# Kernel optimization log

Hardware: AMD Instinct MI355X
Metric: run time of the kernel (lower is better)

The kernel has to match this reference:

```python
import jax, jax.numpy as jnp
import numpy as np

T, H = 2048, 1024
NH, NKV, HD = 8, 2, 128
E, TOPK, NG, TKG = 16, 4, 4, 2
F, FS = 1024, 1024
EPS = 1e-6
ROUTED_SCALE = 2.0
THETA = 10000.0


def _rmsnorm(x, w):
    return x * jax.lax.rsqrt(jnp.mean(x * x, axis=-1, keepdims=True) + EPS) * w


def setup_inputs() -> dict:
    key = jax.random.key(0)
    ks = jax.random.split(key, 12)
    s = 0.02
    return {
        "hidden_states": jax.random.normal(ks[0], (T, H), jnp.float32),
        "residual": jax.random.normal(ks[1], (T, H), jnp.float32),
        "position_ids": jnp.arange(T, dtype=jnp.int32),
        "ln1_w": jnp.ones((H,), jnp.float32),
        "qkv_w": s * jax.random.normal(ks[2], (H, (NH + 2 * NKV) * HD), jnp.float32),
        "qnorm_w": jnp.ones((HD,), jnp.float32),
        "knorm_w": jnp.ones((HD,), jnp.float32),
        "dense_w": s * jax.random.normal(ks[3], (NH * HD, H), jnp.float32),
        "ln2_w": jnp.ones((H,), jnp.float32),
        "gate_w": s * jax.random.normal(ks[4], (H, E), jnp.float32),
        "expert_bias": 0.1 * jax.random.normal(ks[5], (E,), jnp.float32),
        "w13": s * jax.random.normal(ks[6], (E, H, 2 * F), jnp.float32),
        "w2": s * jax.random.normal(ks[7], (E, F, H), jnp.float32),
        "ws_gate_up": s * jax.random.normal(ks[8], (H, 2 * FS), jnp.float32),
        "ws_down": s * jax.random.normal(ks[9], (FS, H), jnp.float32),
    }


def block_forward(hidden_states, residual, position_ids, ln1_w, qkv_w, qnorm_w,
                  knorm_w, dense_w, ln2_w, gate_w, expert_bias, w13, w2,
                  ws_gate_up, ws_down):
    # fused add + RMSNorm (input_layernorm with residual)
    resid = hidden_states + residual
    h = _rmsnorm(resid, ln1_w)

    # --- attention ---
    qkv = h @ qkv_w  # [T, (NH+2*NKV)*HD]
    q = qkv[:, : NH * HD].reshape(T, NH, HD)
    k = qkv[:, NH * HD : (NH + NKV) * HD].reshape(T, NKV, HD)
    v = qkv[:, (NH + NKV) * HD :].reshape(T, NKV, HD)
    q = _rmsnorm(q, qnorm_w)  # qk-norm per head_dim
    k = _rmsnorm(k, knorm_w)

    # neox-style RoPE over full head_dim
    inv_freq = 1.0 / (THETA ** (jnp.arange(0, HD, 2, dtype=jnp.float32) / HD))
    ang = position_ids.astype(jnp.float32)[:, None] * inv_freq[None, :]  # [T, HD/2]
    cos = jnp.cos(ang)[:, None, :]
    sin = jnp.sin(ang)[:, None, :]

    def rope(x):
        x1, x2 = x[..., : HD // 2], x[..., HD // 2 :]
        return jnp.concatenate([x1 * cos - x2 * sin, x2 * cos + x1 * sin], axis=-1)

    q, k = rope(q), rope(k)
    rep = NH // NKV
    kr = jnp.repeat(k, rep, axis=1)  # [T, NH, HD]
    vr = jnp.repeat(v, rep, axis=1)

    scores = jnp.einsum("qhd,khd->hqk", q, kr) * (HD ** -0.5)
    causal = jnp.tril(jnp.ones((T, T), bool))
    scores = jnp.where(causal[None], scores, jnp.finfo(scores.dtype).min)
    probs = jax.nn.softmax(scores, axis=-1)
    ctx = jnp.einsum("hqk,khd->qhd", probs, vr).reshape(T, NH * HD)
    attn_out = ctx @ dense_w

    # fused add + RMSNorm (post_attention_layernorm)
    resid2 = attn_out + resid
    h2 = _rmsnorm(resid2, ln2_w)

    # --- MoE router: sigmoid scoring + correction bias, grouped top-k ---
    logits = h2.astype(jnp.float32) @ gate_w  # router in fp32
    s_scores = jax.nn.sigmoid(logits)  # [T, E]
    sfc = s_scores + expert_bias[None, :]
    gview = sfc.reshape(T, NG, E // NG)
    gscores = jax.lax.top_k(gview, 2)[0].sum(-1)  # sum of top-2 per group
    gidx = jax.lax.top_k(gscores, TKG)[1]  # [T, TKG]
    gmask = jax.nn.one_hot(gidx, NG, dtype=sfc.dtype).sum(1)  # [T, NG]
    smask = jnp.repeat(gmask, E // NG, axis=1)  # [T, E]
    masked = jnp.where(smask > 0, sfc, -jnp.inf)
    topk_idx = jax.lax.top_k(masked, TOPK)[1]  # [T, TOPK]
    topk_w = jnp.take_along_axis(s_scores, topk_idx, axis=1)  # weights w/o bias
    topk_w = topk_w / (topk_w.sum(-1, keepdims=True) + 1e-20)  # renormalize
    combine = (jax.nn.one_hot(topk_idx, E, dtype=topk_w.dtype) * topk_w[..., None]).sum(1)  # [T, E]

    # routed experts (dense-over-experts reference for the grouped GEMM)
    gu = jnp.einsum("th,ehf->tef", h2, w13)  # [T, E, 2F]
    g, u = gu[..., :F], gu[..., F:]
    act = jax.nn.silu(g) * u
    y = jnp.einsum("tef,efh->teh", act, w2)
    routed = jnp.einsum("teh,te->th", y, combine) * ROUTED_SCALE

    # shared expert (SwiGLU MLP)
    su = h2 @ ws_gate_up
    shared = (jax.nn.silu(su[:, :FS]) * su[:, FS:]) @ ws_down

    mlp_out = routed + shared
    return mlp_out, resid2


def reference(hidden_states, residual, position_ids, ln1_w, qkv_w, qnorm_w,
              knorm_w, dense_w, ln2_w, gate_w, expert_bias, w13, w2,
              ws_gate_up, ws_down):
    return block_forward(hidden_states, residual, position_ids, ln1_w, qkv_w,
                         qnorm_w, knorm_w, dense_w, ln2_w, gate_w, expert_bias,
                         w13, w2, ws_gate_up, ws_down)
```

## Files before the change

kernel.cpp:

```cpp
#include <hip/hip_runtime.h>
#include <hip/hip_bf16.h>


#define T_TOK 2048
#define H_DIM 1024
#define NHEAD 8
#define NKVH 2
#define HDIM 128
#define QKV_DIM 1536
#define E_EXP 16
#define TOPKE 4
#define F_DIM 1024
#define FS_DIM 1024
#define NPAIR (T_TOK*TOPKE)
#define EPS_F 1e-6f

#define DEV __device__ __forceinline__

typedef __attribute__((ext_vector_type(4))) float f32x4;
typedef __attribute__((ext_vector_type(8))) short s16x8;

DEV float us2f(unsigned short u){ return __uint_as_float(((unsigned int)u)<<16); }
DEV unsigned short f2us(float f){
  __hip_bfloat16 b = __float2bfloat16(f);
  unsigned short u; __builtin_memcpy(&u,&b,2); return u;
}

DEV void gl2lds16(const void* g, void* l){
  __builtin_amdgcn_global_load_lds(
      (const __attribute__((address_space(1))) void*)g,
      (__attribute__((address_space(3))) void*)l, 16, 0, 0);
}

DEV int crow(int qt){ int a=qt>>2, b=qt&3; return (a+1)*(2*a+b); }

DEV float bred_sum(float v, float* sm){
  #pragma unroll
  for(int o=32;o>0;o>>=1) v += __shfl_down(v,o);
  int w = threadIdx.x>>6, l = threadIdx.x&63;
  __syncthreads();
  if(l==0) sm[w]=v;
  __syncthreads();
  return sm[0]+sm[1]+sm[2]+sm[3];
}

__global__ __launch_bounds__(256) void k_cvt_t(const float* __restrict__ in,
    unsigned short* __restrict__ out, int Kd, int Nd){
  const int z = blockIdx.z;
  const int kb = blockIdx.y*32, nb = blockIdx.x*32;
  __shared__ float Lt[32][33];
  const int tid = threadIdx.x;
  const int r = tid>>3, c4 = (tid&7)*4;
  const float* src = in + (long long)z*Kd*Nd + (long long)(kb+r)*Nd + nb + c4;
  float4 v = *(const float4*)src;
  Lt[r][c4+0]=v.x; Lt[r][c4+1]=v.y; Lt[r][c4+2]=v.z; Lt[r][c4+3]=v.w;
  __syncthreads();
  ushort4 o;
  o.x = f2us(Lt[c4+0][r]); o.y = f2us(Lt[c4+1][r]);
  o.z = f2us(Lt[c4+2][r]); o.w = f2us(Lt[c4+3][r]);
  *(ushort4*)(out + (long long)z*Nd*Kd + (long long)(nb+r)*Kd + kb + c4) = o;
}

template<bool GROUPED, bool GATHER>
__global__ __launch_bounds__(256) void gemm_mfma(
    const unsigned short* __restrict__ A, int lda,
    const unsigned short* __restrict__ Bt, int ldbt, long long bstride,
    unsigned short* __restrict__ C, int ldc,
    const int* __restrict__ rowidx, const int* __restrict__ grpoff,
    int Mdense, int K){
  const int z = blockIdx.z;
  const int rb = GROUPED ? grpoff[z] : 0;
  const int re = GROUPED ? grpoff[z+1] : Mdense;
  const int m0 = rb + blockIdx.y*128;
  if(m0 >= re) return;
  const int n0 = blockIdx.x*128;
  const unsigned short* Bz = Bt + (long long)z*bstride;

  __shared__ unsigned short As[128][32];
  __shared__ unsigned short Bs[128][32];

  const int tid = threadIdx.x;
  const int s0 = tid, s1 = tid+256;
  int gr0 = m0 + (s0>>2), gr1 = m0 + (s1>>2);
  if(GROUPED){ gr0 = min(gr0, re-1); gr1 = min(gr1, re-1); }
  if(GATHER){ gr0 = rowidx[gr0]; gr1 = rowidx[gr1]; }
  const unsigned short* ag0 = A + (long long)gr0*lda + (s0&3)*8;
  const unsigned short* ag1 = A + (long long)gr1*lda + (s1&3)*8;
  const unsigned short* bg0 = Bz + (long long)(n0 + (s0>>2))*ldbt + (s0&3)*8;
  const unsigned short* bg1 = Bz + (long long)(n0 + (s1>>2))*ldbt + (s1&3)*8;
  char* asb = (char*)&As[0][0];
  char* bsb = (char*)&Bs[0][0];
  const int wb = (tid & 192)*16;

  const int w = tid>>6, lane = tid&63;
  const int wm = (w>>1)*64, wn = (w&1)*64;
  const int fr = lane&15, q8 = (lane>>4)*8;

  f32x4 zero = {0.f,0.f,0.f,0.f};
  f32x4 acc[4][4];
  #pragma unroll
  for(int mi=0;mi<4;mi++)
    #pragma unroll
    for(int ni=0;ni<4;ni++) acc[mi][ni]=zero;

  for(int k0=0;k0<K;k0+=32){
    __syncthreads();
    gl2lds16(ag0 + k0, asb + wb);
    gl2lds16(ag1 + k0, asb + 4096 + wb);
    gl2lds16(bg0 + k0, bsb + wb);
    gl2lds16(bg1 + k0, bsb + 4096 + wb);
    __syncthreads();
    s16x8 af[4], bf[4];
    #pragma unroll
    for(int mi=0;mi<4;mi++) af[mi] = *(const s16x8*)&As[wm+mi*16+fr][q8];
    #pragma unroll
    for(int ni=0;ni<4;ni++) bf[ni] = *(const s16x8*)&Bs[wn+ni*16+fr][q8];
    #pragma unroll
    for(int mi=0;mi<4;mi++)
      #pragma unroll
      for(int ni=0;ni<4;ni++)
        acc[mi][ni] = __builtin_amdgcn_mfma_f32_16x16x32_bf16(af[mi], bf[ni], acc[mi][ni], 0,0,0);
  }
  const int q4 = (lane>>4)*4;
  #pragma unroll
  for(int mi=0;mi<4;mi++)
    #pragma unroll
    for(int ni=0;ni<4;ni++){
      const int col = n0 + wn + ni*16 + fr;
      #pragma unroll
      for(int r=0;r<4;r++){
        const int row = m0 + wm + mi*16 + q4 + r;
        if(row < re) C[(long long)row*ldc + col] = f2us(acc[mi][ni][r]);
      }
    }
}

__global__ __launch_bounds__(256) void k_silu(const unsigned short* __restrict__ gu,
    unsigned short* __restrict__ act){
  const int r = blockIdx.x, c = threadIdx.x*4;
  const ushort4 g4 = *(const ushort4*)(gu + (long long)r*2048 + c);
  const ushort4 u4 = *(const ushort4*)(gu + (long long)r*2048 + 1024 + c);
  float g[4] = {us2f(g4.x),us2f(g4.y),us2f(g4.z),us2f(g4.w)};
  float u[4] = {us2f(u4.x),us2f(u4.y),us2f(u4.z),us2f(u4.w)};
  ushort4 o;
  o.x = f2us((g[0]/(1.f+__expf(-g[0])))*u[0]);
  o.y = f2us((g[1]/(1.f+__expf(-g[1])))*u[1]);
  o.z = f2us((g[2]/(1.f+__expf(-g[2])))*u[2]);
  o.w = f2us((g[3]/(1.f+__expf(-g[3])))*u[3]);
  *(ushort4*)(act + (long long)r*1024 + c) = o;
}

__global__ __launch_bounds__(256) void k_add_rmsnorm(const float* __restrict__ hs,
    const float* __restrict__ rs, const float* __restrict__ w,
    float* __restrict__ resid, float* __restrict__ h){
  int t = blockIdx.x, tid = threadIdx.x;
  __shared__ float sm[4];
  const long base = (long)t*H_DIM;
  float x[4]; float ss = 0.f;
  #pragma unroll
  for(int i=0;i<4;i++){
    int c = tid + i*256;
    float v = hs[base+c] + rs[base+c];
    x[i]=v; resid[base+c]=v; ss += v*v;
  }
  float tot = bred_sum(ss, sm);
  float rms = rsqrtf(tot/(float)H_DIM + EPS_F);
  #pragma unroll
  for(int i=0;i<4;i++){
    int c = tid + i*256;
    h[base+c] = x[i]*rms*w[c];
  }
}

template<int EPI_ADD>
__global__ __launch_bounds__(256) void gemm_f32(
    const float* __restrict__ A, int lda,
    const float* __restrict__ B, int ldb,
    float* __restrict__ C, int ldc,
    const float* __restrict__ D, int M, int K){
  const int m0 = blockIdx.y*128;
  const int n0 = blockIdx.x*64;
  __shared__ float As[16][132];
  __shared__ float Bs[16][65];
  float acc[8][4];
  #pragma unroll
  for(int i=0;i<8;i++)
    #pragma unroll
    for(int j=0;j<4;j++) acc[i][j]=0.f;
  const int tid = threadIdx.x;
  const int tx = tid & 15, ty = tid >> 4;
  const int ar = tid >> 1, ac = (tid & 1)*8;
  const int brr = tid >> 4, bc = (tid & 15)*4;
  const float* Aptr = A + (long long)(m0+ar)*lda;
  for(int k0=0;k0<K;k0+=16){
    float4 a0 = *(const float4*)(Aptr + k0 + ac);
    float4 a1 = *(const float4*)(Aptr + k0 + ac + 4);
    float4 bv = *(const float4*)(B + (long long)(k0+brr)*ldb + n0 + bc);
    __syncthreads();
    As[ac+0][ar]=a0.x; As[ac+1][ar]=a0.y; As[ac+2][ar]=a0.z; As[ac+3][ar]=a0.w;
    As[ac+4][ar]=a1.x; As[ac+5][ar]=a1.y; As[ac+6][ar]=a1.z; As[ac+7][ar]=a1.w;
    Bs[brr][bc+0]=bv.x; Bs[brr][bc+1]=bv.y; Bs[brr][bc+2]=bv.z; Bs[brr][bc+3]=bv.w;
    __syncthreads();
    #pragma unroll
    for(int kk=0;kk<16;kk++){
      float a[8], b[4];
      #pragma unroll
      for(int i=0;i<8;i++) a[i]=As[kk][ty*8+i];
      #pragma unroll
      for(int j=0;j<4;j++) b[j]=Bs[kk][tx*4+j];
      #pragma unroll
      for(int i=0;i<8;i++)
        #pragma unroll
        for(int j=0;j<4;j++) acc[i][j] = fmaf(a[i], b[j], acc[i][j]);
    }
  }
  #pragma unroll
  for(int i=0;i<8;i++){
    int r = m0 + ty*8 + i;
    float* crow = C + (long long)r*ldc + n0 + tx*4;
    float4 v = make_float4(acc[i][0],acc[i][1],acc[i][2],acc[i][3]);
    if(EPI_ADD){
      const float4 d = *(const float4*)(D + (long long)r*ldc + n0 + tx*4);
      v.x+=d.x; v.y+=d.y; v.z+=d.z; v.w+=d.w;
    }
    *(float4*)crow = v;
  }
}

__global__ __launch_bounds__(64) void k_qkv_post(const float* __restrict__ qkv,
    const float* __restrict__ qw, const float* __restrict__ kw,
    const int* __restrict__ pos,
    float* __restrict__ qb, float* __restrict__ kb, float* __restrict__ vb){
  int slot = blockIdx.x, t = blockIdx.y, lane = threadIdx.x;
  const float* x = qkv + (long long)t*QKV_DIM + slot*HDIM;
  float x0 = x[lane], x1 = x[lane+64];
  if(slot < 10){
    float ss = x0*x0 + x1*x1;
    #pragma unroll
    for(int o=32;o>0;o>>=1) ss += __shfl_xor(ss,o);
    float rms = rsqrtf(ss/(float)HDIM + EPS_F);
    const float* w = (slot<8)? qw : kw;
    float n0 = x0*rms*w[lane];
    float n1 = x1*rms*w[lane+64];
    float p = (float)pos[t];
    float invf = __expf(-((float)lane/64.f)*9.210340371976184f);
    float ang = p*invf;
    float s = sinf(ang), c = cosf(ang);
    float o0 = n0*c - n1*s;
    float o1 = n1*c + n0*s;
    float* dst = (slot<8)? (qb + ((long long)slot*T_TOK + t)*HDIM)
                         : (kb + ((long long)(slot-8)*T_TOK + t)*HDIM);
    dst[lane]=o0; dst[lane+64]=o1;
  } else {
    float* dst = vb + ((long long)(slot-10)*T_TOK + t)*HDIM;
    dst[lane]=x0; dst[lane+64]=x1;
  }
}

#define FBQ 32
#define FBK 128
__global__ __launch_bounds__(256,2) void k_flash(const float* __restrict__ qb,
    const float* __restrict__ kb, const float* __restrict__ vb,
    float* __restrict__ ctx, float* __restrict__ Op1, float* __restrict__ Op2,
    float* __restrict__ Ml){
  const int b = blockIdx.x;
  const int u0 = (17*b)>>1, u1 = (17*(b+1))>>1;
  const int tid = threadIdx.x;
  const int lane = tid & 63;
  const int w = tid >> 6;
  const int tx = tid & 31;
  const int ty = tid >> 5;
  const int fsw = tx & 7;

  __shared__ float4 smem4[4096];
  char*  smem = (char*)smem4;
  float* Ksf  = (float*)smem;
  float* Psf  = (float*)(smem + 49152);

  const float scale = 0.08838834764831845f;

  int h = u0/544;
  int r = u0 - h*544;
  int qt = 0;
  while(qt < 63 && crow(qt+1) <= r) qt++;
  int kt = r - crow(qt);

  int u = u0;
  while(u < u1){
    const int nkt = (qt>>2) + 1;
    const int q0 = qt * FBQ;
    const int kv = h >> 2;
    const float* kbase = kb + (long long)kv*T_TOK*HDIM;
    const float* vbase = vb + (long long)kv*T_TOK*HDIM;
    const float* qrow0 = qb + ((long long)h*T_TOK + q0 + ty*4)*HDIM;
    const int segN = min(nkt - kt, u1 - u);
    const int ktEnd = kt + segN;

    float m_[4], l_[4], O[4][4];
    #pragma unroll
    for(int qi=0;qi<4;qi++){
      m_[qi] = -1e30f; l_[qi] = 0.f;
      #pragma unroll
      for(int j=0;j<4;j++) O[qi][j] = 0.f;
    }

    for(; kt<ktEnd; kt++){
      const int k0 = kt * FBK;
      __syncthreads();
      {
        const float* kcur = kbase + (long long)k0*HDIM;
        #pragma unroll
        for(int i=0;i<16;i++){
          const int rbase = (w<<5) + (i<<1);
          const int f = (i>>1) & 7;
          const float* src = kcur + (long long)(rbase + (lane>>5))*HDIM
                                  + (((lane&31)^f)<<2);
          gl2lds16(src, smem + rbase*512);
        }
      }
      __syncthreads();

      float s[4][4];
      #pragma unroll
      for(int qi=0;qi<4;qi++)
        #pragma unroll
        for(int ki=0;ki<4;ki++) s[qi][ki] = 0.f;

      #pragma unroll 2
      for(int dc=0; dc<32; dc++){
        float4 qv[4];
        #pragma unroll
        for(int qi=0;qi<4;qi++) qv[qi] = *(const float4*)(qrow0 + qi*HDIM + dc*4);
        float4 kf[4];
        #pragma unroll
        for(int ki=0;ki<4;ki++)
          kf[ki] = *(const float4*)&Ksf[(size_t)(4*tx+ki)*128 + ((dc ^ fsw)<<2)];
        #pragma unroll
        for(int qi=0;qi<4;qi++)
          #pragma unroll
          for(int ki=0;ki<4;ki++){
            s[qi][ki] = fmaf(qv[qi].x, kf[ki].x, s[qi][ki]);
            s[qi][ki] = fmaf(qv[qi].y, kf[ki].y, s[qi][ki]);
            s[qi][ki] = fmaf(qv[qi].z, kf[ki].z, s[qi][ki]);
            s[qi][ki] = fmaf(qv[qi].w, kf[ki].w, s[qi][ki]);
          }
      }

      const bool last = (kt == nkt-1);
      float rm[4];
      #pragma unroll
      for(int qi=0;qi<4;qi++){
        #pragma unroll
        for(int ki=0;ki<4;ki++){
          float v = s[qi][ki]*scale;
          if(last && (k0 + 4*tx + ki > q0 + ty*4 + qi)) v = -1e30f;
          s[qi][ki] = v;
        }
        rm[qi] = fmaxf(fmaxf(s[qi][0],s[qi][1]), fmaxf(s[qi][2],s[qi][3]));
      }
      #pragma unroll
      for(int o=1;o<32;o<<=1){
        #pragma unroll
        for(int qi=0;qi<4;qi++) rm[qi] = fmaxf(rm[qi], __shfl_xor(rm[qi], o));
      }
      float a_[4], rs[4];
      #pragma unroll
      for(int qi=0;qi<4;qi++){
        float mn = fmaxf(m_[qi], rm[qi]);
        a_[qi] = __expf(m_[qi] - mn);
        m_[qi] = mn;
        float rr = 0.f;
        #pragma unroll
        for(int ki=0;ki<4;ki++){ s[qi][ki] = __expf(s[qi][ki] - mn); rr += s[qi][ki]; }
        rs[qi] = rr;
      }
      #pragma unroll
      for(int o=1;o<32;o<<=1){
        #pragma unroll
        for(int qi=0;qi<4;qi++) rs[qi] += __shfl_xor(rs[qi], o);
      }
      #pragma unroll
      for(int qi=0;qi<4;qi++){
        l_[qi] = l_[qi]*a_[qi] + rs[qi];
        #pragma unroll
        for(int j=0;j<4;j++) O[qi][j] *= a_[qi];
      }

      __syncthreads();
      #pragma unroll
      for(int ki=0;ki<4;ki++){
        float4 pv;
        pv.x = s[0][ki]; pv.y = s[1][ki]; pv.z = s[2][ki]; pv.w = s[3][ki];
        *(float4*)&Psf[(size_t)(4*tx+ki)*32 + ((ty ^ fsw)<<2)] = pv;
      }
      __syncthreads();

      const float* vcur = vbase + (long long)k0*HDIM + tx*4;
      #pragma unroll 4
      for(int k=0;k<FBK;k++){
        float4 p4 = *(const float4*)&Psf[(size_t)k*32 + ((ty ^ ((k>>2)&7))<<2)];
        float4 vv = *(const float4*)(vcur + (size_t)k*HDIM);
        O[0][0]=fmaf(p4.x,vv.x,O[0][0]); O[0][1]=fmaf(p4.x,vv.y,O[0][1]);
        O[0][2]=fmaf(p4.x,vv.z,O[0][2]); O[0][3]=fmaf(p4.x,vv.w,O[0][3]);
        O[1][0]=fmaf(p4.y,vv.x,O[1][0]); O[1][1]=fmaf(p4.y,vv.y,O[1][1]);
        O[1][2]=fmaf(p4.y,vv.z,O[1][2]); O[1][3]=fmaf(p4.y,vv.w,O[1][3]);
        O[2][0]=fmaf(p4.z,vv.x,O[2][0]); O[2][1]=fmaf(p4.z,vv.y,O[2][1]);
        O[2][2]=fmaf(p4.z,vv.z,O[2][2]); O[2][3]=fmaf(p4.z,vv.w,O[2][3]);
        O[3][0]=fmaf(p4.w,vv.x,O[3][0]); O[3][1]=fmaf(p4.w,vv.y,O[3][1]);
        O[3][2]=fmaf(p4.w,vv.z,O[3][2]); O[3][3]=fmaf(p4.w,vv.w,O[3][3]);
      }
    }

    {
      const int R = (h<<6) + qt;
      const int S = h*544 + crow(qt);
      const int bS = (2*S+1)/17;
      const int j = b - bS;
      #pragma unroll
      for(int qi=0;qi<4;qi++){
        const int row = ty*4 + qi;
        float4 o4 = make_float4(O[qi][0],O[qi][1],O[qi][2],O[qi][3]);
        if(j==0){
          *(float4*)(ctx + (long long)(q0+row)*(NHEAD*HDIM) + h*HDIM + tx*4) = o4;
        } else if(j==1){
          *(float4*)(Op1 + (long long)R*4096 + row*128 + tx*4) = o4;
        } else {
          *(float4*)(Op2 + (long long)R*4096 + row*128 + tx*4) = o4;
        }
        if(tx==0){
          Ml[((R*3+j)<<6) + row*2 + 0] = m_[qi];
          Ml[((R*3+j)<<6) + row*2 + 1] = l_[qi];
        }
      }
    }

    u += segN;
    if(ktEnd == nkt){ kt = 0; qt++; if(qt == 64){ qt = 0; h++; } }
    else kt = ktEnd;
  }
}

__global__ __launch_bounds__(256) void k_fmerge(float* __restrict__ ctx,
    const float* __restrict__ Op1, const float* __restrict__ Op2,
    const float* __restrict__ Ml){
  const int wv = threadIdx.x>>6, lane = threadIdx.x&63;
  const int gr = blockIdx.x*4 + wv;
  const int R = gr>>5, q = gr&31;
  const int h = R>>6, qt = R&63;
  const int nkt = (qt>>2)+1;
  const int S = h*544 + crow(qt);
  const int bS = (2*S+1)/17;
  const int bE = (2*(S+nkt-1)+1)/17;
  const int parts = bE - bS + 1;
  float* dst = ctx + (long long)(qt*32+q)*(NHEAD*HDIM) + h*HDIM + lane*2;
  float2 o0 = *(float2*)dst;
  const float* mlb = Ml + ((R*3)<<6) + q*2;
  const float m0 = mlb[0], l0 = mlb[1];
  float ox, oy;
  if(parts == 1){
    float inv = 1.f/l0;
    ox = o0.x*inv; oy = o0.y*inv;
  } else {
    const float m1 = mlb[64], l1 = mlb[65];
    float2 o1 = *(const float2*)(Op1 + (long long)R*4096 + q*128 + lane*2);
    if(parts == 2){
      float mx = fmaxf(m0,m1);
      float a0 = __expf(m0-mx), a1 = __expf(m1-mx);
      float inv = 1.f/(l0*a0 + l1*a1);
      ox = (o0.x*a0 + o1.x*a1)*inv;
      oy = (o0.y*a0 + o1.y*a1)*inv;
    } else {
      const float m2 = mlb[128], l2 = mlb[129];
      float2 o2 = *(const float2*)(Op2 + (long long)R*4096 + q*128 + lane*2);
      float mx = fmaxf(fmaxf(m0,m1),m2);
      float a0 = __expf(m0-mx), a1 = __expf(m1-mx), a2 = __expf(m2-mx);
      float inv = 1.f/(l0*a0 + l1*a1 + l2*a2);
      ox = (o0.x*a0 + o1.x*a1 + o2.x*a2)*inv;
      oy = (o0.y*a0 + o1.y*a1 + o2.y*a2)*inv;
    }
  }
  dst[0] = ox; dst[1] = oy;
}

__global__ __launch_bounds__(256) void k_rms2(const float* __restrict__ r2,
    const float* __restrict__ w, float* __restrict__ h2f,
    unsigned short* __restrict__ h2b){
  int t = blockIdx.x, tid = threadIdx.x;
  __shared__ float sm[4];
  const long base = (long)t*H_DIM;
  float x[4]; float ss=0.f;
  #pragma unroll
  for(int i=0;i<4;i++){
    int c = tid+i*256;
    float v = r2[base+c];
    x[i]=v; ss += v*v;
  }
  float tot = bred_sum(ss, sm);
  float rms = rsqrtf(tot/(float)H_DIM + EPS_F);
  #pragma unroll
  for(int i=0;i<4;i++){
    int c = tid+i*256;
    float v = x[i]*rms*w[c];
    h2f[base+c] = v;
    h2b[base+c] = f2us(v);
  }
}

__global__ __launch_bounds__(256) void k_router(const float* __restrict__ h2,
    const float* __restrict__ gw, const float* __restrict__ eb,
    int* __restrict__ topk_idx, float* __restrict__ topk_w, int* __restrict__ counts){
  int t = blockIdx.x, tid = threadIdx.x;
  int e = tid & 15, seg = tid >> 4;
  const float* hrow = h2 + (long long)t*H_DIM;
  float part = 0.f;
  #pragma unroll 4
  for(int i=0;i<64;i++){
    int hh = seg*64 + i;
    part += hrow[hh]*gw[hh*E_EXP + e];
  }
  __shared__ float pm[16][17];
  __shared__ float sS[16], sfc[16];
  pm[seg][e] = part;
  __syncthreads();
  if(tid < 16){
    float l = 0.f;
    #pragma unroll
    for(int s=0;s<16;s++) l += pm[s][tid];
    float sg = 1.f/(1.f+expf(-l));
    sS[tid]=sg; sfc[tid]=sg+eb[tid];
  }
  __syncthreads();
  if(tid==0){
    float gs[4];
    #pragma unroll
    for(int g=0; g<4; g++){
      float m1=-1e30f, m2=-1e30f;
      for(int j=0;j<4;j++){
        float v=sfc[g*4+j];
        if(v>m1){ m2=m1; m1=v; } else if(v>m2){ m2=v; }
      }
      gs[g]=m1+m2;
    }
    int g1=0; for(int g=1;g<4;g++) if(gs[g]>gs[g1]) g1=g;
    int g2=-1; for(int g=0;g<4;g++){ if(g==g1) continue; if(g2<0||gs[g]>gs[g2]) g2=g; }
    bool taken[16];
    #pragma unroll
    for(int i=0;i<16;i++) taken[i]=false;
    int idx[4];
    for(int j=0;j<4;j++){
      int best=-1; float bv=-1e30f;
      for(int i=0;i<16;i++){
        int g=i>>2;
        if(g!=g1 && g!=g2) continue;
        if(taken[i]) continue;
        if(best<0 || sfc[i]>bv){ best=i; bv=sfc[i]; }
      }
      taken[best]=true; idx[j]=best;
    }
    float w[4]; float s=0.f;
    #pragma unroll
    for(int j=0;j<4;j++){ w[j]=sS[idx[j]]; s+=w[j]; }
    s += 1e-20f;
    #pragma unroll
    for(int j=0;j<4;j++){
      topk_idx[t*4+j]=idx[j];
      topk_w[t*4+j]=w[j]/s;
      atomicAdd(&counts[idx[j]],1);
    }
  }
}

__global__ void k_zero(int* __restrict__ counts){ if(threadIdx.x<16) counts[threadIdx.x]=0; }

__global__ void k_scan(const int* __restrict__ counts, int* __restrict__ offs, int* __restrict__ cursor){
  if(threadIdx.x==0){
    int s=0;
    for(int e2=0;e2<16;e2++){ offs[e2]=s; cursor[e2]=s; s+=counts[e2]; }
    offs[16]=s;
  }
}

__global__ __launch_bounds__(256) void k_scatter(const int* __restrict__ topk_idx,
    int* __restrict__ cursor, int* __restrict__ pair_tok, int* __restrict__ tok2pair){
  int i = blockIdx.x*256 + threadIdx.x;
  int e = topk_idx[i];
  int pos = atomicAdd(&cursor[e],1);
  pair_tok[pos] = i>>2;
  tok2pair[i] = pos;
}

__global__ __launch_bounds__(256) void k_combine(const unsigned short* __restrict__ y,
    const unsigned short* __restrict__ sout, const int* __restrict__ tok2pair,
    const float* __restrict__ topk_w, float* __restrict__ out0){
  int t = blockIdx.x, tid = threadIdx.x;
  int p[4]; float w[4];
  #pragma unroll
  for(int j=0;j<4;j++){ p[j]=tok2pair[t*4+j]; w[j]=topk_w[t*4+j]*2.0f; }
  const long base = (long)t*H_DIM;
  #pragma unroll
  for(int i=0;i<4;i++){
    int c = tid + i*256;
    float v = us2f(sout[base+c]);
    #pragma unroll
    for(int j=0;j<4;j++) v += w[j]*us2f(y[(long long)p[j]*H_DIM + c]);
    out0[base+c] = v;
  }
}

extern "C" void kernel_launch(void* const* d_in, const int* in_sizes, int n_in,
                              void* d_out, int out_size, void* d_ws, size_t ws_size,
                              hipStream_t stream) {
  const float* hs   = (const float*)d_in[0];
  const float* rsd  = (const float*)d_in[1];
  const int*   pos  = (const int*)d_in[2];
  const float* ln1  = (const float*)d_in[3];
  const float* qkvw = (const float*)d_in[4];
  const float* qnw  = (const float*)d_in[5];
  const float* knw  = (const float*)d_in[6];
  const float* dw   = (const float*)d_in[7];
  const float* ln2  = (const float*)d_in[8];
  const float* gw   = (const float*)d_in[9];
  const float* eb   = (const float*)d_in[10];
  const float* w13  = (const float*)d_in[11];
  const float* w2   = (const float*)d_in[12];
  const float* wsgu = (const float*)d_in[13];
  const float* wsd  = (const float*)d_in[14];
  float* out0 = (float*)d_out;
  float* out1 = out0 + (size_t)T_TOK*H_DIM;

  char* W = (char*)d_ws;
  float* resid = (float*)(W + 0);
  float* h     = (float*)(W + 8388608);
  float* ctx   = h;
  float* qkv   = (float*)(W + 16777216);
  float* qb    = (float*)(W + 29360128);
  float* h2f   = (float*)(W + 37748736);
  float* kb    = (float*)(W + 46137344);
  float* vb    = (float*)(W + 48234496);
  float* Op1   = (float*)(W + 16777216);
  float* Ml    = (float*)(W + 25165824);
  float* Op2   = (float*)(W + 37748736);
  unsigned short* gu    = (unsigned short*)(W + 8388608);
  unsigned short* ybuf  = (unsigned short*)(W + 8388608);
  unsigned short* sgu   = (unsigned short*)(W + 16777216);
  unsigned short* sact  = (unsigned short*)(W + 0);
  unsigned short* sout  = (unsigned short*)(W + 46137344);
  unsigned short* h2b   = (unsigned short*)(W + 50331648);
  unsigned short* act   = (unsigned short*)(W + 54525952);
  unsigned short* w13t  = (unsigned short*)(W + 71303168);
  unsigned short* w2t   = (unsigned short*)(W + 138412032);
  unsigned short* wsgut = (unsigned short*)(W + 171966464);
  unsigned short* wsdt  = (unsigned short*)(W + 176160768);
  float* topkw = (float*)(W + 178257920);
  int* topki   = (int*)(W + 178290688);
  int* ptok    = (int*)(W + 178323456);
  int* t2p     = (int*)(W + 178356224);
  int* cnt     = (int*)(W + 178388992);
  int* offs    = (int*)(W + 178389056);
  int* cur     = (int*)(W + 178389184);

  k_cvt_t<<<dim3(64,32,16), 256, 0, stream>>>(w13,  w13t,  1024, 2048);
  k_cvt_t<<<dim3(32,32,16), 256, 0, stream>>>(w2,   w2t,   1024, 1024);
  k_cvt_t<<<dim3(64,32,1),  256, 0, stream>>>(wsgu, wsgut, 1024, 2048);
  k_cvt_t<<<dim3(32,32,1),  256, 0, stream>>>(wsd,  wsdt,  1024, 1024);
  k_add_rmsnorm<<<T_TOK, 256, 0, stream>>>(hs, rsd, ln1, resid, h);
  gemm_f32<0><<<dim3(QKV_DIM/64, T_TOK/128), 256, 0, stream>>>(
      h, H_DIM, qkvw, QKV_DIM, qkv, QKV_DIM, nullptr, T_TOK, H_DIM);
  k_qkv_post<<<dim3(12, T_TOK), 64, 0, stream>>>(qkv, qnw, knw, pos, qb, kb, vb);
  k_flash<<<512, 256, 0, stream>>>(qb, kb, vb, ctx, Op1, Op2, Ml);
  k_fmerge<<<4096, 256, 0, stream>>>(ctx, Op1, Op2, Ml);
  gemm_f32<1><<<dim3(H_DIM/64, T_TOK/128), 256, 0, stream>>>(
      ctx, NHEAD*HDIM, dw, H_DIM, out1, H_DIM, resid, T_TOK, NHEAD*HDIM);
  k_rms2<<<T_TOK, 256, 0, stream>>>(out1, ln2, h2f, h2b);
  k_zero<<<1, 64, 0, stream>>>(cnt);
  k_router<<<T_TOK, 256, 0, stream>>>(h2f, gw, eb, topki, topkw, cnt);
  k_scan<<<1, 64, 0, stream>>>(cnt, offs, cur);
  k_scatter<<<NPAIR/256, 256, 0, stream>>>(topki, cur, ptok, t2p);
  gemm_mfma<false,false><<<dim3(16,16,1), 256, 0, stream>>>(
      h2b, 1024, wsgut, 1024, 0, sgu, 2048, nullptr, nullptr, T_TOK, 1024);
  k_silu<<<T_TOK, 256, 0, stream>>>(sgu, sact);
  gemm_mfma<false,false><<<dim3(8,16,1), 256, 0, stream>>>(
      sact, 1024, wsdt, 1024, 0, sout, 1024, nullptr, nullptr, T_TOK, 1024);
  gemm_mfma<true,true><<<dim3(16,64,16), 256, 0, stream>>>(
      h2b, 1024, w13t, 1024, (long long)2048*1024, gu, 2048, ptok, offs, 0, 1024);
  k_silu<<<NPAIR, 256, 0, stream>>>(gu, act);
  gemm_mfma<true,false><<<dim3(8,64,16), 256, 0, stream>>>(
      act, 1024, w2t, 1024, (long long)1024*1024, ybuf, 1024, nullptr, offs, 0, 1024);
  k_combine<<<T_TOK, 256, 0, stream>>>(ybuf, sout, t2p, topkw, out0);
}
```

Before: 1.060 ms.

## Replace FP32 SIMT attention projections with split-bf16 three-pass MFMA GEMMs

```diff
diff --git a/kernel.cpp b/kernel.cpp
--- a/kernel.cpp
+++ b/kernel.cpp
@@ -61,6 +61,28 @@
   *(ushort4*)(out + (long long)z*Nd*Kd + (long long)(nb+r)*Kd + kb + c4) = o;
 }
 
+__global__ __launch_bounds__(256) void k_cvt_t3(const float* __restrict__ in,
+    unsigned short* __restrict__ oh, unsigned short* __restrict__ ol,
+    int Kd, int Nd){
+  const int kb = blockIdx.y*32, nb = blockIdx.x*32;
+  __shared__ float Lt[32][33];
+  const int tid = threadIdx.x;
+  const int r = tid>>3, c4 = (tid&7)*4;
+  const float* src = in + (long long)(kb+r)*Nd + nb + c4;
+  float4 v = *(const float4*)src;
+  Lt[r][c4+0]=v.x; Lt[r][c4+1]=v.y; Lt[r][c4+2]=v.z; Lt[r][c4+3]=v.w;
+  __syncthreads();
+  ushort4 h4, l4;
+  float f;
+  f = Lt[c4+0][r]; h4.x = f2us(f); l4.x = f2us(f - us2f(h4.x));
+  f = Lt[c4+1][r]; h4.y = f2us(f); l4.y = f2us(f - us2f(h4.y));
+  f = Lt[c4+2][r]; h4.z = f2us(f); l4.z = f2us(f - us2f(h4.z));
+  f = Lt[c4+3][r]; h4.w = f2us(f); l4.w = f2us(f - us2f(h4.w));
+  const long long ob = (long long)(nb+r)*Kd + kb + c4;
+  *(ushort4*)(oh + ob) = h4;
+  *(ushort4*)(ol + ob) = l4;
+}
+
 template<bool GROUPED, bool GATHER>
 __global__ __launch_bounds__(256) void gemm_mfma(
     const unsigned short* __restrict__ A, int lda,
@@ -135,6 +157,89 @@
     }
 }
 
+template<int EPI_ADD>
+__global__ __launch_bounds__(256) void gemm_mfma3(
+    const unsigned short* __restrict__ Ah, const unsigned short* __restrict__ Al, int lda,
+    const unsigned short* __restrict__ Bh, const unsigned short* __restrict__ Bl, int ldbt,
+    float* __restrict__ C, int ldc, const float* __restrict__ D, int K){
+  const int m0 = blockIdx.y*128;
+  const int n0 = blockIdx.x*128;
+
+  __shared__ unsigned short Ash[128][32];
+  __shared__ unsigned short Asl[128][32];
+  __shared__ unsigned short Bsh[128][32];
+  __shared__ unsigned short Bsl[128][32];
+
+  const int tid = threadIdx.x;
+  const int s0 = tid, s1 = tid+256;
+  const long long ar0 = (long long)(m0 + (s0>>2))*lda + (s0&3)*8;
+  const long long ar1 = (long long)(m0 + (s1>>2))*lda + (s1&3)*8;
+  const long long br0 = (long long)(n0 + (s0>>2))*ldbt + (s0&3)*8;
+  const long long br1 = (long long)(n0 + (s1>>2))*ldbt + (s1&3)*8;
+  char* ahb = (char*)&Ash[0][0];
+  char* alb = (char*)&Asl[0][0];
+  char* bhb = (char*)&Bsh[0][0];
+  char* blb = (char*)&Bsl[0][0];
+  const int wb = (tid & 192)*16;
+
+  const int w = tid>>6, lane = tid&63;
+  const int wm = (w>>1)*64, wn = (w&1)*64;
+  const int fr = lane&15, q8 = (lane>>4)*8;
+
+  f32x4 zero = {0.f,0.f,0.f,0.f};
+  f32x4 acc[4][4];
+  #pragma unroll
+  for(int mi=0;mi<4;mi++)
+    #pragma unroll
+    for(int ni=0;ni<4;ni++) acc[mi][ni]=zero;
+
+  for(int k0=0;k0<K;k0+=32){
+    __syncthreads();
+    gl2lds16(Ah + ar0 + k0, ahb + wb);
+    gl2lds16(Ah + ar1 + k0, ahb + 4096 + wb);
+    gl2lds16(Al + ar0 + k0, alb + wb);
+    gl2lds16(Al + ar1 + k0, alb + 4096 + wb);
+    gl2lds16(Bh + br0 + k0, bhb + wb);
+    gl2lds16(Bh + br1 + k0, bhb + 4096 + wb);
+    gl2lds16(Bl + br0 + k0, blb + wb);
+    gl2lds16(Bl + br1 + k0, blb + 4096 + wb);
+    __syncthreads();
+    s16x8 afh[4], afl[4], bfh[4], bfl[4];
+    #pragma unroll
+    for(int mi=0;mi<4;mi++){
+      afh[mi] = *(const s16x8*)&Ash[wm+mi*16+fr][q8];
+      afl[mi] = *(const s16x8*)&Asl[wm+mi*16+fr][q8];
+    }
+    #pragma unroll
+    for(int ni=0;ni<4;ni++){
+      bfh[ni] = *(const s16x8*)&Bsh[wn+ni*16+fr][q8];
+      bfl[ni] = *(const s16x8*)&Bsl[wn+ni*16+fr][q8];
+    }
+    #pragma unroll
+    for(int mi=0;mi<4;mi++)
+      #pragma unroll
+      for(int ni=0;ni<4;ni++){
+        acc[mi][ni] = __builtin_amdgcn_mfma_f32_16x16x32_bf16(afh[mi], bfh[ni], acc[mi][ni], 0,0,0);
+        acc[mi][ni] = __builtin_amdgcn_mfma_f32_16x16x32_bf16(afh[mi], bfl[ni], acc[mi][ni], 0,0,0);
+        acc[mi][ni] = __builtin_amdgcn_mfma_f32_16x16x32_bf16(afl[mi], bfh[ni], acc[mi][ni], 0,0,0);
+      }
+  }
+  const int q4 = (lane>>4)*4;
+  #pragma unroll
+  for(int mi=0;mi<4;mi++)
+    #pragma unroll
+    for(int ni=0;ni<4;ni++){
+      const int col = n0 + wn + ni*16 + fr;
+      #pragma unroll
+      for(int r=0;r<4;r++){
+        const int row = m0 + wm + mi*16 + q4 + r;
+        float v = acc[mi][ni][r];
+        if(EPI_ADD) v += D[(long long)row*ldc + col];
+        C[(long long)row*ldc + col] = v;
+      }
+    }
+}
+
 __global__ __launch_bounds__(256) void k_silu(const unsigned short* __restrict__ gu,
     unsigned short* __restrict__ act){
   const int r = blockIdx.x, c = threadIdx.x*4;
@@ -152,7 +257,8 @@
 
 __global__ __launch_bounds__(256) void k_add_rmsnorm(const float* __restrict__ hs,
     const float* __restrict__ rs, const float* __restrict__ w,
-    float* __restrict__ resid, float* __restrict__ h){
+    float* __restrict__ resid, unsigned short* __restrict__ ah,
+    unsigned short* __restrict__ al){
   int t = blockIdx.x, tid = threadIdx.x;
   __shared__ float sm[4];
   const long base = (long)t*H_DIM;
@@ -168,62 +274,10 @@
   #pragma unroll
   for(int i=0;i<4;i++){
     int c = tid + i*256;
-    h[base+c] = x[i]*rms*w[c];
-  }
-}
-
-template<int EPI_ADD>
-__global__ __launch_bounds__(256) void gemm_f32(
-    const float* __restrict__ A, int lda,
-    const float* __restrict__ B, int ldb,
-    float* __restrict__ C, int ldc,
-    const float* __restrict__ D, int M, int K){
-  const int m0 = blockIdx.y*128;
-  const int n0 = blockIdx.x*64;
-  __shared__ float As[16][132];
-  __shared__ float Bs[16][65];
-  float acc[8][4];
-  #pragma unroll
-  for(int i=0;i<8;i++)
-    #pragma unroll
-    for(int j=0;j<4;j++) acc[i][j]=0.f;
-  const int tid = threadIdx.x;
-  const int tx = tid & 15, ty = tid >> 4;
-  const int ar = tid >> 1, ac = (tid & 1)*8;
-  const int brr = tid >> 4, bc = (tid & 15)*4;
-  const float* Aptr = A + (long long)(m0+ar)*lda;
-  for(int k0=0;k0<K;k0+=16){
-    float4 a0 = *(const float4*)(Aptr + k0 + ac);
-    float4 a1 = *(const float4*)(Aptr + k0 + ac + 4);
-    float4 bv = *(const float4*)(B + (long long)(k0+brr)*ldb + n0 + bc);
-    __syncthreads();
-    As[ac+0][ar]=a0.x; As[ac+1][ar]=a0.y; As[ac+2][ar]=a0.z; As[ac+3][ar]=a0.w;
-    As[ac+4][ar]=a1.x; As[ac+5][ar]=a1.y; As[ac+6][ar]=a1.z; As[ac+7][ar]=a1.w;
-    Bs[brr][bc+0]=bv.x; Bs[brr][bc+1]=bv.y; Bs[brr][bc+2]=bv.z; Bs[brr][bc+3]=bv.w;
-    __syncthreads();
-    #pragma unroll
-    for(int kk=0;kk<16;kk++){
-      float a[8], b[4];
-      #pragma unroll
-      for(int i=0;i<8;i++) a[i]=As[kk][ty*8+i];
-      #pragma unroll
-      for(int j=0;j<4;j++) b[j]=Bs[kk][tx*4+j];
-      #pragma unroll
-      for(int i=0;i<8;i++)
-        #pragma unroll
-        for(int j=0;j<4;j++) acc[i][j] = fmaf(a[i], b[j], acc[i][j]);
-    }
-  }
-  #pragma unroll
-  for(int i=0;i<8;i++){
-    int r = m0 + ty*8 + i;
-    float* crow = C + (long long)r*ldc + n0 + tx*4;
-    float4 v = make_float4(acc[i][0],acc[i][1],acc[i][2],acc[i][3]);
-    if(EPI_ADD){
-      const float4 d = *(const float4*)(D + (long long)r*ldc + n0 + tx*4);
-      v.x+=d.x; v.y+=d.y; v.z+=d.z; v.w+=d.w;
-    }
-    *(float4*)crow = v;
+    float v = x[i]*rms*w[c];
+    unsigned short hh = f2us(v);
+    ah[base+c] = hh;
+    al[base+c] = f2us(v - us2f(hh));
   }
 }
 
@@ -440,9 +494,10 @@
   }
 }
 
-__global__ __launch_bounds__(256) void k_fmerge(float* __restrict__ ctx,
+__global__ __launch_bounds__(256) void k_fmerge(const float* __restrict__ ctx,
     const float* __restrict__ Op1, const float* __restrict__ Op2,
-    const float* __restrict__ Ml){
+    const float* __restrict__ Ml, unsigned short* __restrict__ ch,
+    unsigned short* __restrict__ cl){
   const int wv = threadIdx.x>>6, lane = threadIdx.x&63;
   const int gr = blockIdx.x*4 + wv;
   const int R = gr>>5, q = gr&31;
@@ -452,8 +507,8 @@
   const int bS = (2*S+1)/17;
   const int bE = (2*(S+nkt-1)+1)/17;
   const int parts = bE - bS + 1;
-  float* dst = ctx + (long long)(qt*32+q)*(NHEAD*HDIM) + h*HDIM + lane*2;
-  float2 o0 = *(float2*)dst;
+  const float* src0 = ctx + (long long)(qt*32+q)*(NHEAD*HDIM) + h*HDIM + lane*2;
+  float2 o0 = *(const float2*)src0;
   const float* mlb = Ml + ((R*3)<<6) + q*2;
   const float m0 = mlb[0], l0 = mlb[1];
   float ox, oy;
@@ -479,7 +534,10 @@
       oy = (o0.y*a0 + o1.y*a1 + o2.y*a2)*inv;
     }
   }
-  dst[0] = ox; dst[1] = oy;
+  const long long idx = (long long)(qt*32+q)*(NHEAD*HDIM) + h*HDIM + lane*2;
+  unsigned short hx = f2us(ox), hy = f2us(oy);
+  ch[idx] = hx;   cl[idx] = f2us(ox - us2f(hx));
+  ch[idx+1] = hy; cl[idx+1] = f2us(oy - us2f(hy));
 }
 
 __global__ __launch_bounds__(256) void k_rms2(const float* __restrict__ r2,
@@ -630,8 +688,9 @@
 
   char* W = (char*)d_ws;
   float* resid = (float*)(W + 0);
-  float* h     = (float*)(W + 8388608);
-  float* ctx   = h;
+  unsigned short* ah = (unsigned short*)(W + 8388608);
+  unsigned short* al = (unsigned short*)(W + 12582912);
+  float* ctx   = (float*)(W + 8388608);
   float* qkv   = (float*)(W + 16777216);
   float* qb    = (float*)(W + 29360128);
   float* h2f   = (float*)(W + 37748736);
@@ -640,6 +699,12 @@
   float* Op1   = (float*)(W + 16777216);
   float* Ml    = (float*)(W + 25165824);
   float* Op2   = (float*)(W + 37748736);
+  unsigned short* cth = (unsigned short*)(W + 29360128);
+  unsigned short* ctl = (unsigned short*)(W + 33554432);
+  unsigned short* qwt_h = (unsigned short*)(W + 37748736);
+  unsigned short* qwt_l = (unsigned short*)(W + 40894464);
+  unsigned short* dwt_h = (unsigned short*)(W + 50331648);
+  unsigned short* dwt_l = (unsigned short*)(W + 52428800);
   unsigned short* gu    = (unsigned short*)(W + 8388608);
   unsigned short* ybuf  = (unsigned short*)(W + 8388608);
   unsigned short* sgu   = (unsigned short*)(W + 16777216);
@@ -663,14 +728,16 @@
   k_cvt_t<<<dim3(32,32,16), 256, 0, stream>>>(w2,   w2t,   1024, 1024);
   k_cvt_t<<<dim3(64,32,1),  256, 0, stream>>>(wsgu, wsgut, 1024, 2048);
   k_cvt_t<<<dim3(32,32,1),  256, 0, stream>>>(wsd,  wsdt,  1024, 1024);
-  k_add_rmsnorm<<<T_TOK, 256, 0, stream>>>(hs, rsd, ln1, resid, h);
-  gemm_f32<0><<<dim3(QKV_DIM/64, T_TOK/128), 256, 0, stream>>>(
-      h, H_DIM, qkvw, QKV_DIM, qkv, QKV_DIM, nullptr, T_TOK, H_DIM);
+  k_cvt_t3<<<dim3(48,32,1), 256, 0, stream>>>(qkvw, qwt_h, qwt_l, 1024, 1536);
+  k_cvt_t3<<<dim3(32,32,1), 256, 0, stream>>>(dw,   dwt_h, dwt_l, 1024, 1024);
+  k_add_rmsnorm<<<T_TOK, 256, 0, stream>>>(hs, rsd, ln1, resid, ah, al);
+  gemm_mfma3<0><<<dim3(QKV_DIM/128, T_TOK/128), 256, 0, stream>>>(
+      ah, al, 1024, qwt_h, qwt_l, 1024, qkv, QKV_DIM, nullptr, 1024);
   k_qkv_post<<<dim3(12, T_TOK), 64, 0, stream>>>(qkv, qnw, knw, pos, qb, kb, vb);
   k_flash<<<512, 256, 0, stream>>>(qb, kb, vb, ctx, Op1, Op2, Ml);
-  k_fmerge<<<4096, 256, 0, stream>>>(ctx, Op1, Op2, Ml);
-  gemm_f32<1><<<dim3(H_DIM/64, T_TOK/128), 256, 0, stream>>>(
-      ctx, NHEAD*HDIM, dw, H_DIM, out1, H_DIM, resid, T_TOK, NHEAD*HDIM);
+  k_fmerge<<<4096, 256, 0, stream>>>(ctx, Op1, Op2, Ml, cth, ctl);
+  gemm_mfma3<1><<<dim3(H_DIM/128, T_TOK/128), 256, 0, stream>>>(
+      cth, ctl, 1024, dwt_h, dwt_l, 1024, out1, H_DIM, resid, 1024);
   k_rms2<<<T_TOK, 256, 0, stream>>>(out1, ln2, h2f, h2b);
   k_zero<<<1, 64, 0, stream>>>(cnt);
   k_router<<<T_TOK, 256, 0, stream>>>(h2f, gw, eb, topki, topkw, cnt);
```

Measured after the change: 935.8 us. 1.13x faster.
